# Optimization experiments

Hardware: AMD Instinct MI355X
Metric: run time of the kernel (lower is better)

## Reference

```python
import jax, jax.numpy as jnp
import numpy as np

N, IN_CAPS, OUT_CAPS, IN_LEN, OUT_LEN = 64, 256, 128, 16, 32
NUM_ITERATIONS = 3


def _squash(t, axis=-1):
    # scale * t / sqrt(||t||^2) with scale = ||t||^2 / (1 + ||t||^2)
    sq = jnp.sum(t * t, axis=axis, keepdims=True)
    return (sq / (1.0 + sq)) * t / jnp.sqrt(sq)


def setup_inputs() -> dict:
    key = jax.random.key(0)
    k1, k2 = jax.random.split(key)
    x = jax.random.normal(k1, (N, IN_CAPS, IN_LEN), dtype=jnp.float32)
    weight = jax.random.normal(k2, (OUT_CAPS, IN_CAPS, IN_LEN, OUT_LEN), dtype=jnp.float32)
    return {"x": x, "weight": weight}


def reference(x, weight):
    # priors: [out_caps, N, in_caps, out_len]  (torch keeps an extra singleton dim)
    priors = jnp.einsum('nik,oikl->onil', x, weight)
    logits = jnp.zeros_like(priors)
    outputs = None
    for i in range(NUM_ITERATIONS):
        # torch softmax(dim=2) == softmax over the in_caps axis
        probs = jax.nn.softmax(logits, axis=2)
        s = jnp.sum(probs * priors, axis=2, keepdims=True)  # [O, N, 1, L]
        outputs = _squash(s, axis=-1)
        if i != NUM_ITERATIONS - 1:
            # delta broadcasts over out_len, as in the torch code
            logits = logits + jnp.sum(priors * outputs, axis=-1, keepdims=True)
    # squeeze routing dim, transpose to [N, out_caps, out_len]
    return jnp.transpose(outputs[:, :, 0, :], (1, 0, 2))
```

## Files before the change

kernel.cpp:

```cpp
#include <hip/hip_runtime.h>


#define ICAPS 256
#define OCAPS 128
#define WS_WH 0ull
#define WS_WL 33554432ull
#define WS_XH 67108864ull
#define WS_XL 67633152ull
#define WS_NEED 68157440ull

typedef __attribute__((ext_vector_type(8))) short s16x8;
typedef __attribute__((ext_vector_type(16))) float f32x16;

__device__ inline unsigned bfbits(float f) {
    unsigned u = __float_as_uint(f);
    return (u + 0x7FFFu + ((u >> 16) & 1u)) & 0xFFFF0000u;
}

__global__ __launch_bounds__(256)
void caps_prep(const float* __restrict__ x, const float* __restrict__ w,
               unsigned char* __restrict__ ws) {
    const int wv = threadIdx.x >> 6, lane = threadIdx.x & 63;
    unsigned* WH = (unsigned*)(ws + WS_WH);
    unsigned* WL = (unsigned*)(ws + WS_WL);
    unsigned* XH = (unsigned*)(ws + WS_XH);
    unsigned* XL = (unsigned*)(ws + WS_XL);

    float f[8];
    if (blockIdx.x < 8192) {
        const int id = blockIdx.x * 4 + wv;
        const int l = lane & 31, kb = (lane >> 5) * 8;
        const float* src = w + ((size_t)id * 16 + kb) * 32 + l;
        #pragma unroll
        for (int j = 0; j < 8; ++j) f[j] = src[j * 32];
        unsigned h[4], g[4];
        #pragma unroll
        for (int c = 0; c < 4; ++c) {
            unsigned b0 = bfbits(f[2 * c]), b1 = bfbits(f[2 * c + 1]);
            h[c] = (b0 >> 16) | (b1 & 0xFFFF0000u);
            float l0 = f[2 * c] - __uint_as_float(b0);
            float l1 = f[2 * c + 1] - __uint_as_float(b1);
            g[c] = (bfbits(l0) >> 16) | (bfbits(l1) & 0xFFFF0000u);
        }
        const size_t o4 = (size_t)(id * 64 + lane) * 4;
        *(uint4*)(WH + o4) = make_uint4(h[0], h[1], h[2], h[3]);
        *(uint4*)(WL + o4) = make_uint4(g[0], g[1], g[2], g[3]);
    } else {
        const int id = (blockIdx.x - 8192) * 4 + wv;
        const int nh = id >> 8, i = id & 255;
        const int np = lane & 31, kb = (lane >> 5) * 8;
        const float* src = x + ((size_t)(nh * 32 + np) * ICAPS + i) * 16 + kb;
        float4 a = *(const float4*)src, b = *(const float4*)(src + 4);
        f[0] = a.x; f[1] = a.y; f[2] = a.z; f[3] = a.w;
        f[4] = b.x; f[5] = b.y; f[6] = b.z; f[7] = b.w;
        unsigned h[4], g[4];
        #pragma unroll
        for (int c = 0; c < 4; ++c) {
            unsigned b0 = bfbits(f[2 * c]), b1 = bfbits(f[2 * c + 1]);
            h[c] = (b0 >> 16) | (b1 & 0xFFFF0000u);
            float l0 = f[2 * c] - __uint_as_float(b0);
            float l1 = f[2 * c + 1] - __uint_as_float(b1);
            g[c] = (bfbits(l0) >> 16) | (bfbits(l1) & 0xFFFF0000u);
        }
        const size_t o4 = (size_t)(id * 64 + lane) * 4;
        *(uint4*)(XH + o4) = make_uint4(h[0], h[1], h[2], h[3]);
        *(uint4*)(XL + o4) = make_uint4(g[0], g[1], g[2], g[3]);
    }
}

__global__ __launch_bounds__(512)
void caps_main(const unsigned char* __restrict__ ws, float* __restrict__ out) {
    __shared__ float lg[ICAPS * 32];
    __shared__ float slab[8 * 1280];
    __shared__ float svv[32 * 33];
    __shared__ float zz[8 * 32];
    __shared__ float zinv[32];

    const int t = threadIdx.x, wv = t >> 6, lane = t & 63;
    const int o = blockIdx.x & 127, nh = blockIdx.x >> 7;
    const int n = lane & 31, half = lane >> 5;

    const s16x8* WHp = (const s16x8*)(ws + WS_WH) + (size_t)o * ICAPS * 64 + lane;
    const s16x8* WLp = (const s16x8*)(ws + WS_WL) + (size_t)o * ICAPS * 64 + lane;
    const s16x8* XHp = (const s16x8*)(ws + WS_XH) + (size_t)nh * ICAPS * 64 + lane;
    const s16x8* XLp = (const s16x8*)(ws + WS_XL) + (size_t)nh * ICAPS * 64 + lane;

    float vr[16];
    const int ibase = wv * 32;

    for (int pass = 0; pass < 3; ++pass) {
        float uacc[16];
        #pragma unroll
        for (int r = 0; r < 16; ++r) uacc[r] = 0.f;
        float z = 0.f;

        for (int ii = 0; ii < 32; ++ii) {
            const int i = ibase + ii;
            const s16x8 ah = WHp[(size_t)i * 64];
            const s16x8 al = WLp[(size_t)i * 64];
            const s16x8 bh = XHp[(size_t)i * 64];
            const s16x8 bl = XLp[(size_t)i * 64];
            f32x16 P = {};
            P = __builtin_amdgcn_mfma_f32_32x32x16_bf16(al, bh, P, 0, 0, 0);
            P = __builtin_amdgcn_mfma_f32_32x32x16_bf16(ah, bl, P, 0, 0, 0);
            P = __builtin_amdgcn_mfma_f32_32x32x16_bf16(ah, bh, P, 0, 0, 0);

            if (pass == 0) {
                #pragma unroll
                for (int r = 0; r < 16; ++r) uacc[r] += P[r];
            } else {
                float da = P[0] * vr[0];
                float db = P[8] * vr[8];
                #pragma unroll
                for (int r = 1; r < 8; ++r) {
                    da = fmaf(P[r], vr[r], da);
                    db = fmaf(P[r + 8], vr[r + 8], db);
                }
                float d = da + db;
                d += __shfl_xor(d, 32);
                if (pass == 1) {
                    if (half == 0) lg[i * 32 + n] = d;
                } else {
                    d += lg[i * 32 + n];
                }
                const float e = __expf(d);
                z += e;
                #pragma unroll
                for (int r = 0; r < 16; ++r) uacc[r] = fmaf(e, P[r], uacc[r]);
            }
        }

        #pragma unroll
        for (int c = 0; c < 4; ++c)
            *(float4*)(&slab[wv * 1280 + lane * 20 + c * 4]) =
                make_float4(uacc[4 * c], uacc[4 * c + 1], uacc[4 * c + 2], uacc[4 * c + 3]);
        if (pass > 0 && half == 0) zz[wv * 32 + n] = z;
        __syncthreads();

        #pragma unroll
        for (int hh = 0; hh < 2; ++hh) {
            const int e = t + hh * 512;
            const int lw = e >> 4, r = e & 15;
            float s = 0.f;
            #pragma unroll
            for (int w8 = 0; w8 < 8; ++w8) s += slab[w8 * 1280 + lw * 20 + r];
            const int nn = lw & 31, ll = (r & 3) + 8 * (r >> 2) + 4 * (lw >> 5);
            svv[nn * 33 + ll] = s;
        }
        if (t < 32) {
            if (pass == 0) zinv[t] = 1.0f / 256.0f;
            else {
                float zs = 0.f;
                #pragma unroll
                for (int w8 = 0; w8 < 8; ++w8) zs += zz[w8 * 32 + t];
                zinv[t] = 1.0f / zs;
            }
        }
        __syncthreads();

        {
            const int nq = t >> 4, sub = t & 15;
            const float a = svv[nq * 33 + sub] * zinv[nq];
            const float b = svv[nq * 33 + sub + 16] * zinv[nq];
            float sq = a * a + b * b;
            #pragma unroll
            for (int m = 1; m < 16; m <<= 1) sq += __shfl_xor(sq, m, 16);
            const float sc = sqrtf(sq) / (1.0f + sq);
            if (pass == 2) {
                const int ng = nh * 32 + nq;
                out[((size_t)ng * OCAPS + o) * 32 + sub] = a * sc;
                out[((size_t)ng * OCAPS + o) * 32 + sub + 16] = b * sc;
            } else {
                svv[nq * 33 + sub] = a * sc;
                svv[nq * 33 + sub + 16] = b * sc;
            }
        }
        if (pass < 2) {
            __syncthreads();
            #pragma unroll
            for (int r = 0; r < 16; ++r) {
                const int l = (r & 3) + 8 * (r >> 2) + 4 * half;
                vr[r] = svv[n * 33 + l];
            }
        }
    }
}

#define KLEN  16
#define LLEN  32
#define TN    16
#define LGS   257
#define XROW  20
#define XIST  (TN * XROW + 4)
#define SVS   33
#define RBS   33
#define NSTG  32
#define NSTEP (ICAPS / NSTG)

__global__ __launch_bounds__(512, 2)
void caps_route_fb(const float* __restrict__ xg_all,
                   const float* __restrict__ wg_all,
                   float* __restrict__ out) {
    __shared__ float lg[TN * LGS];
    __shared__ float xt[NSTG * XIST];
    __shared__ float sv[TN * SVS];
    __shared__ float zz[8][TN];
    __shared__ float zinv[TN];

    const int t   = threadIdx.x;
    const int o   = blockIdx.x & 127;
    const int n0  = (blockIdx.x >> 7) * TN;
    const int isp = t >> 4;
    const int lb  = (t >> 2) & 3;
    const int nb  = t & 3;
    const int l0  = lb * 8;

    const float* xg = xg_all + (size_t)n0 * ICAPS * KLEN;
    const float* wg = wg_all + (size_t)o * ICAPS * KLEN * LLEN;

    for (int pass = 0; pass < 3; ++pass) {
        float u[4][8];
        float zq[4] = {0.f, 0.f, 0.f, 0.f};
        #pragma unroll
        for (int q = 0; q < 4; ++q)
            #pragma unroll
            for (int r = 0; r < 8; ++r) u[q][r] = 0.f;

        for (int st = 0; st < NSTEP; ++st) {
            const int i0 = st * NSTG;
            __syncthreads();
            #pragma unroll
            for (int j = 0; j < 4; ++j) {
                const int g   = j * 512 + t;
                const int n   = g >> 7;
                const int rem = g & 127;
                const int il  = rem >> 2;
                const int k4c = rem & 3;
                *(float4*)(&xt[il * XIST + n * XROW + k4c * 4]) =
                    *(const float4*)(xg + (size_t)(n * ICAPS + i0 + il) * KLEN + k4c * 4);
            }
            __syncthreads();

            const int i = i0 + isp;
            const float* wp = wg + (size_t)i * (KLEN * LLEN) + l0;
            const float* xp = &xt[isp * XIST];
            float P[4][8];
            #pragma unroll
            for (int q = 0; q < 4; ++q)
                #pragma unroll
                for (int r = 0; r < 8; ++r) P[q][r] = 0.f;

            #pragma unroll
            for (int k4 = 0; k4 < 4; ++k4) {
                float xq[4][4];
                #pragma unroll
                for (int q = 0; q < 4; ++q)
                    *(float4*)(&xq[q][0]) = *(const float4*)(xp + (nb + 4 * q) * XROW + k4 * 4);
                #pragma unroll
                for (int kk = 0; kk < 4; ++kk) {
                    const int k = k4 * 4 + kk;
                    const float4 wa = *(const float4*)(wp + k * LLEN);
                    const float4 wb = *(const float4*)(wp + k * LLEN + 4);
                    #pragma unroll
                    for (int q = 0; q < 4; ++q) {
                        const float xv = xq[q][kk];
                        P[q][0] = fmaf(xv, wa.x, P[q][0]);
                        P[q][1] = fmaf(xv, wa.y, P[q][1]);
                        P[q][2] = fmaf(xv, wa.z, P[q][2]);
                        P[q][3] = fmaf(xv, wa.w, P[q][3]);
                        P[q][4] = fmaf(xv, wb.x, P[q][4]);
                        P[q][5] = fmaf(xv, wb.y, P[q][5]);
                        P[q][6] = fmaf(xv, wb.z, P[q][6]);
                        P[q][7] = fmaf(xv, wb.w, P[q][7]);
                    }
                }
            }

            if (pass == 0) {
                #pragma unroll
                for (int q = 0; q < 4; ++q)
                    #pragma unroll
                    for (int r = 0; r < 8; ++r) u[q][r] += P[q][r];
            } else {
                #pragma unroll
                for (int q = 0; q < 4; ++q) {
                    const float* vp = &sv[(nb + 4 * q) * SVS + l0];
                    float d = P[q][0] * vp[0] + P[q][1] * vp[1] + P[q][2] * vp[2] + P[q][3] * vp[3]
                            + P[q][4] * vp[4] + P[q][5] * vp[5] + P[q][6] * vp[6] + P[q][7] * vp[7];
                    d += __shfl_xor(d, 4);
                    d += __shfl_xor(d, 8);
                    float lnew = d;
                    if (pass == 2) lnew += lg[(nb + 4 * q) * LGS + i];
                    else if (lb == 0) lg[(nb + 4 * q) * LGS + i] = lnew;
                    const float e = __expf(lnew);
                    zq[q] += e;
                    #pragma unroll
                    for (int r = 0; r < 8; ++r) u[q][r] = fmaf(e, P[q][r], u[q][r]);
                }
            }
        }

        #pragma unroll
        for (int q = 0; q < 4; ++q) {
            #pragma unroll
            for (int r = 0; r < 8; ++r) {
                float v = u[q][r];
                v += __shfl_xor(v, 16);
                v += __shfl_xor(v, 32);
                u[q][r] = v;
            }
            float zv = zq[q];
            zv += __shfl_xor(zv, 16);
            zv += __shfl_xor(zv, 32);
            zq[q] = zv;
        }
        __syncthreads();
        {
            const int wvv = t >> 6, lane = t & 63;
            if (lane < 16) {
                float* rb = &xt[wvv * (16 * RBS) + lane * RBS];
                #pragma unroll
                for (int q = 0; q < 4; ++q)
                    #pragma unroll
                    for (int r = 0; r < 8; ++r) rb[q * 8 + r] = u[q][r];
            }
            if (pass > 0 && lane < 4) {
                #pragma unroll
                for (int q = 0; q < 4; ++q) zz[wvv][lane + 4 * q] = zq[q];
            }
        }
        __syncthreads();
        {
            const int low4 = t >> 5, qr = t & 31;
            const int qq = qr >> 3, rr = qr & 7;
            const int lbb = low4 >> 2, nbb = low4 & 3;
            float ssum = 0.f;
            #pragma unroll
            for (int w8 = 0; w8 < 8; ++w8) ssum += xt[w8 * (16 * RBS) + low4 * RBS + qr];
            sv[(nbb + 4 * qq) * SVS + lbb * 8 + rr] = ssum;
        }
        if (t < TN) {
            if (pass == 0) zinv[t] = 1.0f / 256.0f;
            else {
                float zs = 0.f;
                #pragma unroll
                for (int w8 = 0; w8 < 8; ++w8) zs += zz[w8][t];
                zinv[t] = 1.0f / zs;
            }
        }
        __syncthreads();
        {
            const int n = t >> 5, l = t & 31;
            const float val = sv[n * SVS + l] * zinv[n];
            float sq = val * val;
            #pragma unroll
            for (int m = 1; m < 32; m <<= 1) sq += __shfl_xor(sq, m, 32);
            const float sc = sqrtf(sq) / (1.0f + sq);
            if (pass == 2)
                out[((size_t)(n0 + n) * OCAPS + o) * LLEN + l] = val * sc;
            else
                sv[n * SVS + l] = val * sc;
        }
    }
}

extern "C" void kernel_launch(void* const* d_in, const int* in_sizes, int n_in,
                              void* d_out, int out_size, void* d_ws, size_t ws_size,
                              hipStream_t stream) {
    const float* x = (const float*)d_in[0];
    const float* w = (const float*)d_in[1];
    float* outp = (float*)d_out;
    if (ws_size >= WS_NEED) {
        caps_prep<<<dim3(8320), dim3(256), 0, stream>>>(x, w, (unsigned char*)d_ws);
        caps_main<<<dim3(256), dim3(512), 0, stream>>>((const unsigned char*)d_ws, outp);
    } else {
        caps_route_fb<<<dim3(512), dim3(512), 0, stream>>>(x, w, outp);
    }
}
```

Measured before the change: 151.4 us.

## Interleave hi/lo bf16 split storage and software-pipeline MFMA loads two caps per step

Stores the high and low bf16 halves of each weight and input fragment next to each other, so each lane fetches one contiguous 32-byte chunk instead of reading from two separate arrays. The main loop now processes two input capsules per iteration with two independent MFMA accumulator chains. It also prefetches the next pair's fragments into registers while the current MFMAs run, hiding global load latency. The prep kernel moves to 512-thread blocks. The costs are higher register use from the double buffers, which may lower occupancy, and pass 0 now reorders the fp32 summation.

```diff
diff --git a/kernel.cpp b/kernel.cpp
--- a/kernel.cpp
+++ b/kernel.cpp
@@ -3,10 +3,8 @@
 
 #define ICAPS 256
 #define OCAPS 128
-#define WS_WH 0ull
-#define WS_WL 33554432ull
-#define WS_XH 67108864ull
-#define WS_XL 67633152ull
+#define WS_WC 0ull
+#define WS_XC 67108864ull
 #define WS_NEED 68157440ull
 
 typedef __attribute__((ext_vector_type(8))) short s16x8;
@@ -17,20 +15,18 @@
     return (u + 0x7FFFu + ((u >> 16) & 1u)) & 0xFFFF0000u;
 }
 
-__global__ __launch_bounds__(256)
+__global__ __launch_bounds__(512)
 void caps_prep(const float* __restrict__ x, const float* __restrict__ w,
                unsigned char* __restrict__ ws) {
     const int wv = threadIdx.x >> 6, lane = threadIdx.x & 63;
-    unsigned* WH = (unsigned*)(ws + WS_WH);
-    unsigned* WL = (unsigned*)(ws + WS_WL);
-    unsigned* XH = (unsigned*)(ws + WS_XH);
-    unsigned* XL = (unsigned*)(ws + WS_XL);
+    uint4* WC = (uint4*)(ws + WS_WC);
+    uint4* XC = (uint4*)(ws + WS_XC);
+    const int gid = blockIdx.x * 8 + wv;
 
     float f[8];
-    if (blockIdx.x < 8192) {
-        const int id = blockIdx.x * 4 + wv;
+    if (gid < 32768) {
         const int l = lane & 31, kb = (lane >> 5) * 8;
-        const float* src = w + ((size_t)id * 16 + kb) * 32 + l;
+        const float* src = w + ((size_t)gid * 16 + kb) * 32 + l;
         #pragma unroll
         for (int j = 0; j < 8; ++j) f[j] = src[j * 32];
         unsigned h[4], g[4];
@@ -42,15 +38,16 @@
             float l1 = f[2 * c + 1] - __uint_as_float(b1);
             g[c] = (bfbits(l0) >> 16) | (bfbits(l1) & 0xFFFF0000u);
         }
-        const size_t o4 = (size_t)(id * 64 + lane) * 4;
-        *(uint4*)(WH + o4) = make_uint4(h[0], h[1], h[2], h[3]);
-        *(uint4*)(WL + o4) = make_uint4(g[0], g[1], g[2], g[3]);
+        const size_t idx = ((size_t)gid * 64 + lane) * 2;
+        WC[idx]     = make_uint4(h[0], h[1], h[2], h[3]);
+        WC[idx + 1] = make_uint4(g[0], g[1], g[2], g[3]);
     } else {
-        const int id = (blockIdx.x - 8192) * 4 + wv;
+        const int id = gid - 32768;
         const int nh = id >> 8, i = id & 255;
         const int np = lane & 31, kb = (lane >> 5) * 8;
         const float* src = x + ((size_t)(nh * 32 + np) * ICAPS + i) * 16 + kb;
-        float4 a = *(const float4*)src, b = *(const float4*)(src + 4);
+        const float4 a = *(const float4*)src;
+        const float4 b = *(const float4*)(src + 4);
         f[0] = a.x; f[1] = a.y; f[2] = a.z; f[3] = a.w;
         f[4] = b.x; f[5] = b.y; f[6] = b.z; f[7] = b.w;
         unsigned h[4], g[4];
@@ -62,9 +59,9 @@
             float l1 = f[2 * c + 1] - __uint_as_float(b1);
             g[c] = (bfbits(l0) >> 16) | (bfbits(l1) & 0xFFFF0000u);
         }
-        const size_t o4 = (size_t)(id * 64 + lane) * 4;
-        *(uint4*)(XH + o4) = make_uint4(h[0], h[1], h[2], h[3]);
-        *(uint4*)(XL + o4) = make_uint4(g[0], g[1], g[2], g[3]);
+        const size_t idx = ((size_t)id * 64 + lane) * 2;
+        XC[idx]     = make_uint4(h[0], h[1], h[2], h[3]);
+        XC[idx + 1] = make_uint4(g[0], g[1], g[2], g[3]);
     }
 }
 
@@ -80,10 +77,8 @@
     const int o = blockIdx.x & 127, nh = blockIdx.x >> 7;
     const int n = lane & 31, half = lane >> 5;
 
-    const s16x8* WHp = (const s16x8*)(ws + WS_WH) + (size_t)o * ICAPS * 64 + lane;
-    const s16x8* WLp = (const s16x8*)(ws + WS_WL) + (size_t)o * ICAPS * 64 + lane;
-    const s16x8* XHp = (const s16x8*)(ws + WS_XH) + (size_t)nh * ICAPS * 64 + lane;
-    const s16x8* XLp = (const s16x8*)(ws + WS_XL) + (size_t)nh * ICAPS * 64 + lane;
+    const s16x8* Wp = (const s16x8*)(ws + WS_WC) + ((size_t)o * ICAPS * 64 + lane) * 2;
+    const s16x8* Xp = (const s16x8*)(ws + WS_XC) + ((size_t)nh * ICAPS * 64 + lane) * 2;
 
     float vr[16];
     const int ibase = wv * 32;
@@ -94,39 +89,82 @@
         for (int r = 0; r < 16; ++r) uacc[r] = 0.f;
         float z = 0.f;
 
-        for (int ii = 0; ii < 32; ++ii) {
-            const int i = ibase + ii;
-            const s16x8 ah = WHp[(size_t)i * 64];
-            const s16x8 al = WLp[(size_t)i * 64];
-            const s16x8 bh = XHp[(size_t)i * 64];
-            const s16x8 bl = XLp[(size_t)i * 64];
-            f32x16 P = {};
-            P = __builtin_amdgcn_mfma_f32_32x32x16_bf16(al, bh, P, 0, 0, 0);
-            P = __builtin_amdgcn_mfma_f32_32x32x16_bf16(ah, bl, P, 0, 0, 0);
-            P = __builtin_amdgcn_mfma_f32_32x32x16_bf16(ah, bh, P, 0, 0, 0);
-
-            if (pass == 0) {
-                #pragma unroll
-                for (int r = 0; r < 16; ++r) uacc[r] += P[r];
-            } else {
-                float da = P[0] * vr[0];
-                float db = P[8] * vr[8];
-                #pragma unroll
-                for (int r = 1; r < 8; ++r) {
-                    da = fmaf(P[r], vr[r], da);
-                    db = fmaf(P[r + 8], vr[r + 8], db);
-                }
-                float d = da + db;
-                d += __shfl_xor(d, 32);
-                if (pass == 1) {
-                    if (half == 0) lg[i * 32 + n] = d;
-                } else {
-                    d += lg[i * 32 + n];
-                }
-                const float e = __expf(d);
-                z += e;
-                #pragma unroll
-                for (int r = 0; r < 16; ++r) uacc[r] = fmaf(e, P[r], uacc[r]);
+        s16x8 C[8], Nx[8];
+        {
+            const size_t b0 = (size_t)ibase * 128;
+            C[0] = Wp[b0];       C[1] = Wp[b0 + 1];
+            C[2] = Xp[b0];       C[3] = Xp[b0 + 1];
+            C[4] = Wp[b0 + 128]; C[5] = Wp[b0 + 129];
+            C[6] = Xp[b0 + 128]; C[7] = Xp[b0 + 129];
+        }
+
+        if (pass == 0) {
+            f32x16 Pa = {}, Pb = {};
+            for (int bb = 0; bb < 16; ++bb) {
+                if (bb < 15) {
+                    const size_t bn = (size_t)(ibase + 2 * (bb + 1)) * 128;
+                    Nx[0] = Wp[bn];       Nx[1] = Wp[bn + 1];
+                    Nx[2] = Xp[bn];       Nx[3] = Xp[bn + 1];
+                    Nx[4] = Wp[bn + 128]; Nx[5] = Wp[bn + 129];
+                    Nx[6] = Xp[bn + 128]; Nx[7] = Xp[bn + 129];
+                }
+                Pa = __builtin_amdgcn_mfma_f32_32x32x16_bf16(C[1], C[2], Pa, 0, 0, 0);
+                Pb = __builtin_amdgcn_mfma_f32_32x32x16_bf16(C[5], C[6], Pb, 0, 0, 0);
+                Pa = __builtin_amdgcn_mfma_f32_32x32x16_bf16(C[0], C[3], Pa, 0, 0, 0);
+                Pb = __builtin_amdgcn_mfma_f32_32x32x16_bf16(C[4], C[7], Pb, 0, 0, 0);
+                Pa = __builtin_amdgcn_mfma_f32_32x32x16_bf16(C[0], C[2], Pa, 0, 0, 0);
+                Pb = __builtin_amdgcn_mfma_f32_32x32x16_bf16(C[4], C[6], Pb, 0, 0, 0);
+                if (bb < 15) {
+                    #pragma unroll
+                    for (int j = 0; j < 8; ++j) C[j] = Nx[j];
+                }
+            }
+            #pragma unroll
+            for (int r = 0; r < 16; ++r) uacc[r] = Pa[r] + Pb[r];
+        } else {
+            for (int bb = 0; bb < 16; ++bb) {
+                if (bb < 15) {
+                    const size_t bn = (size_t)(ibase + 2 * (bb + 1)) * 128;
+                    Nx[0] = Wp[bn];       Nx[1] = Wp[bn + 1];
+                    Nx[2] = Xp[bn];       Nx[3] = Xp[bn + 1];
+                    Nx[4] = Wp[bn + 128]; Nx[5] = Wp[bn + 129];
+                    Nx[6] = Xp[bn + 128]; Nx[7] = Xp[bn + 129];
+                }
+                f32x16 P0 = {}, P1 = {};
+                P0 = __builtin_amdgcn_mfma_f32_32x32x16_bf16(C[1], C[2], P0, 0, 0, 0);
+                P1 = __builtin_amdgcn_mfma_f32_32x32x16_bf16(C[5], C[6], P1, 0, 0, 0);
+                P0 = __builtin_amdgcn_mfma_f32_32x32x16_bf16(C[0], C[3], P0, 0, 0, 0);
+                P1 = __builtin_amdgcn_mfma_f32_32x32x16_bf16(C[4], C[7], P1, 0, 0, 0);
+                P0 = __builtin_amdgcn_mfma_f32_32x32x16_bf16(C[0], C[2], P0, 0, 0, 0);
+                P1 = __builtin_amdgcn_mfma_f32_32x32x16_bf16(C[4], C[6], P1, 0, 0, 0);
+
+                #pragma unroll
+                for (int j = 0; j < 2; ++j) {
+                    const f32x16& P = j ? P1 : P0;
+                    const int i = ibase + bb * 2 + j;
+                    float da = P[0] * vr[0];
+                    float db = P[8] * vr[8];
+                    #pragma unroll
+                    for (int r = 1; r < 8; ++r) {
+                        da = fmaf(P[r], vr[r], da);
+                        db = fmaf(P[r + 8], vr[r + 8], db);
+                    }
+                    float d = da + db;
+                    d += __shfl_xor(d, 32);
+                    if (pass == 1) {
+                        if (half == 0) lg[i * 32 + n] = d;
+                    } else {
+                        d += lg[i * 32 + n];
+                    }
+                    const float e = __expf(d);
+                    z += e;
+                    #pragma unroll
+                    for (int r = 0; r < 16; ++r) uacc[r] = fmaf(e, P[r], uacc[r]);
+                }
+                if (bb < 15) {
+                    #pragma unroll
+                    for (int j = 0; j < 8; ++j) C[j] = Nx[j];
+                }
             }
         }
 
@@ -232,12 +270,12 @@
             #pragma unroll
             for (int j = 0; j < 4; ++j) {
                 const int g   = j * 512 + t;
-                const int n   = g >> 7;
+                const int nn  = g >> 7;
                 const int rem = g & 127;
                 const int il  = rem >> 2;
                 const int k4c = rem & 3;
-                *(float4*)(&xt[il * XIST + n * XROW + k4c * 4]) =
-                    *(const float4*)(xg + (size_t)(n * ICAPS + i0 + il) * KLEN + k4c * 4);
+                *(float4*)(&xt[il * XIST + nn * XROW + k4c * 4]) =
+                    *(const float4*)(xg + (size_t)(nn * ICAPS + i0 + il) * KLEN + k4c * 4);
             }
             __syncthreads();
 
@@ -350,16 +388,16 @@
         }
         __syncthreads();
         {
-            const int n = t >> 5, l = t & 31;
-            const float val = sv[n * SVS + l] * zinv[n];
+            const int nn = t >> 5, l = t & 31;
+            const float val = sv[nn * SVS + l] * zinv[nn];
             float sq = val * val;
             #pragma unroll
             for (int m = 1; m < 32; m <<= 1) sq += __shfl_xor(sq, m, 32);
             const float sc = sqrtf(sq) / (1.0f + sq);
             if (pass == 2)
-                out[((size_t)(n0 + n) * OCAPS + o) * LLEN + l] = val * sc;
+                out[((size_t)(n0 + nn) * OCAPS + o) * LLEN + l] = val * sc;
             else
-                sv[n * SVS + l] = val * sc;
+                sv[nn * SVS + l] = val * sc;
         }
     }
 }
@@ -371,7 +409,7 @@
     const float* w = (const float*)d_in[1];
     float* outp = (float*)d_out;
     if (ws_size >= WS_NEED) {
-        caps_prep<<<dim3(8320), dim3(256), 0, stream>>>(x, w, (unsigned char*)d_ws);
+        caps_prep<<<dim3(4160), dim3(512), 0, stream>>>(x, w, (unsigned char*)d_ws);
         caps_main<<<dim3(256), dim3(512), 0, stream>>>((const unsigned char*)d_ws, outp);
     } else {
         caps_route_fb<<<dim3(512), dim3(512), 0, stream>>>(x, w, outp);
```

Result: no change. 151.5 us (+0.1%).

## Split weights to bf16 hi/lo inside main kernel, drop weight prep pass

Applied to the files above, without the earlier changes.

Removes the separate pass that converted the 64MB fp32 weight tensor into bf16 hi/lo workspace arrays. The main kernel now reads fp32 weights directly, splits them in registers with truncation and byte-perm, and double-buffers loads over groups of four input capsules. Only x is still pre-split, into a single interleaved buffer. Pass 0 now accumulates into two MFMA accumulators and launch bounds request two blocks per CU. The cost is that weights are re-read and re-split in every routing pass (3x fp32 reads), more register pressure, and the hi part uses truncation instead of round-to-nearest.

```diff
diff --git a/kernel.cpp b/kernel.cpp
--- a/kernel.cpp
+++ b/kernel.cpp
@@ -3,73 +3,52 @@
 
 #define ICAPS 256
 #define OCAPS 128
-#define WS_WH 0ull
-#define WS_WL 33554432ull
-#define WS_XH 67108864ull
-#define WS_XL 67633152ull
-#define WS_NEED 68157440ull
+#define WS_NEED 1048576ull
 
 typedef __attribute__((ext_vector_type(8))) short s16x8;
 typedef __attribute__((ext_vector_type(16))) float f32x16;
 
-__device__ inline unsigned bfbits(float f) {
-    unsigned u = __float_as_uint(f);
-    return (u + 0x7FFFu + ((u >> 16) & 1u)) & 0xFFFF0000u;
-}
-
-__global__ __launch_bounds__(256)
-void caps_prep(const float* __restrict__ x, const float* __restrict__ w,
-               unsigned char* __restrict__ ws) {
+union u4s8 { unsigned u[4]; s16x8 v; };
+
+__device__ inline void split8(const float* f, s16x8& hi, s16x8& lo) {
+    u4s8 H, L;
+    #pragma unroll
+    for (int c = 0; c < 4; ++c) {
+        const unsigned u0 = __float_as_uint(f[2 * c]);
+        const unsigned u1 = __float_as_uint(f[2 * c + 1]);
+        H.u[c] = __builtin_amdgcn_perm(u1, u0, 0x07060302u);
+        const float h0 = __uint_as_float(u0 & 0xFFFF0000u);
+        const float h1 = __uint_as_float(u1 & 0xFFFF0000u);
+        const unsigned l0 = __float_as_uint(f[2 * c] - h0);
+        const unsigned l1 = __float_as_uint(f[2 * c + 1] - h1);
+        L.u[c] = __builtin_amdgcn_perm(l1, l0, 0x07060302u);
+    }
+    hi = H.v; lo = L.v;
+}
+
+__global__ __launch_bounds__(512)
+void caps_prep_x(const float* __restrict__ x, unsigned char* __restrict__ ws) {
     const int wv = threadIdx.x >> 6, lane = threadIdx.x & 63;
-    unsigned* WH = (unsigned*)(ws + WS_WH);
-    unsigned* WL = (unsigned*)(ws + WS_WL);
-    unsigned* XH = (unsigned*)(ws + WS_XH);
-    unsigned* XL = (unsigned*)(ws + WS_XL);
-
+    const int id = blockIdx.x * 8 + wv;
+    const int nh = id >> 8, i = id & 255;
+    const int np = lane & 31, kb = (lane >> 5) * 8;
+    const float* src = x + ((size_t)(nh * 32 + np) * ICAPS + i) * 16 + kb;
     float f[8];
-    if (blockIdx.x < 8192) {
-        const int id = blockIdx.x * 4 + wv;
-        const int l = lane & 31, kb = (lane >> 5) * 8;
-        const float* src = w + ((size_t)id * 16 + kb) * 32 + l;
-        #pragma unroll
-        for (int j = 0; j < 8; ++j) f[j] = src[j * 32];
-        unsigned h[4], g[4];
-        #pragma unroll
-        for (int c = 0; c < 4; ++c) {
-            unsigned b0 = bfbits(f[2 * c]), b1 = bfbits(f[2 * c + 1]);
-            h[c] = (b0 >> 16) | (b1 & 0xFFFF0000u);
-            float l0 = f[2 * c] - __uint_as_float(b0);
-            float l1 = f[2 * c + 1] - __uint_as_float(b1);
-            g[c] = (bfbits(l0) >> 16) | (bfbits(l1) & 0xFFFF0000u);
-        }
-        const size_t o4 = (size_t)(id * 64 + lane) * 4;
-        *(uint4*)(WH + o4) = make_uint4(h[0], h[1], h[2], h[3]);
-        *(uint4*)(WL + o4) = make_uint4(g[0], g[1], g[2], g[3]);
-    } else {
-        const int id = (blockIdx.x - 8192) * 4 + wv;
-        const int nh = id >> 8, i = id & 255;
-        const int np = lane & 31, kb = (lane >> 5) * 8;
-        const float* src = x + ((size_t)(nh * 32 + np) * ICAPS + i) * 16 + kb;
-        float4 a = *(const float4*)src, b = *(const float4*)(src + 4);
-        f[0] = a.x; f[1] = a.y; f[2] = a.z; f[3] = a.w;
-        f[4] = b.x; f[5] = b.y; f[6] = b.z; f[7] = b.w;
-        unsigned h[4], g[4];
-        #pragma unroll
-        for (int c = 0; c < 4; ++c) {
-            unsigned b0 = bfbits(f[2 * c]), b1 = bfbits(f[2 * c + 1]);
-            h[c] = (b0 >> 16) | (b1 & 0xFFFF0000u);
-            float l0 = f[2 * c] - __uint_as_float(b0);
-            float l1 = f[2 * c + 1] - __uint_as_float(b1);
-            g[c] = (bfbits(l0) >> 16) | (bfbits(l1) & 0xFFFF0000u);
-        }
-        const size_t o4 = (size_t)(id * 64 + lane) * 4;
-        *(uint4*)(XH + o4) = make_uint4(h[0], h[1], h[2], h[3]);
-        *(uint4*)(XL + o4) = make_uint4(g[0], g[1], g[2], g[3]);
-    }
-}
-
-__global__ __launch_bounds__(512)
-void caps_main(const unsigned char* __restrict__ ws, float* __restrict__ out) {
+    const float4 a = *(const float4*)src;
+    const float4 b = *(const float4*)(src + 4);
+    f[0] = a.x; f[1] = a.y; f[2] = a.z; f[3] = a.w;
+    f[4] = b.x; f[5] = b.y; f[6] = b.z; f[7] = b.w;
+    s16x8 hi, lo;
+    split8(f, hi, lo);
+    s16x8* XC = (s16x8*)ws;
+    const size_t idx = ((size_t)id * 64 + lane) * 2;
+    XC[idx] = hi;
+    XC[idx + 1] = lo;
+}
+
+__global__ __launch_bounds__(512, 2)
+void caps_main(const float* __restrict__ w, const unsigned char* __restrict__ ws,
+               float* __restrict__ out) {
     __shared__ float lg[ICAPS * 32];
     __shared__ float slab[8 * 1280];
     __shared__ float svv[32 * 33];
@@ -80,35 +59,60 @@
     const int o = blockIdx.x & 127, nh = blockIdx.x >> 7;
     const int n = lane & 31, half = lane >> 5;
 
-    const s16x8* WHp = (const s16x8*)(ws + WS_WH) + (size_t)o * ICAPS * 64 + lane;
-    const s16x8* WLp = (const s16x8*)(ws + WS_WL) + (size_t)o * ICAPS * 64 + lane;
-    const s16x8* XHp = (const s16x8*)(ws + WS_XH) + (size_t)nh * ICAPS * 64 + lane;
-    const s16x8* XLp = (const s16x8*)(ws + WS_XL) + (size_t)nh * ICAPS * 64 + lane;
+    const float* wg = w + (size_t)o * (ICAPS * 512) + (lane >> 5) * 256 + (lane & 31);
+    const s16x8* Xp = (const s16x8*)ws + ((size_t)nh * ICAPS * 64 + lane) * 2;
 
     float vr[16];
     const int ibase = wv * 32;
 
+    auto LOADB = [&](int ib, float (&Wb)[4][8], s16x8 (&Xb)[4][2]) {
+        #pragma unroll
+        for (int j = 0; j < 4; ++j) {
+            const float* wp = wg + (size_t)(ib + j) * 512;
+            #pragma unroll
+            for (int k = 0; k < 8; ++k) Wb[j][k] = wp[k * 32];
+            Xb[j][0] = Xp[(size_t)(ib + j) * 128];
+            Xb[j][1] = Xp[(size_t)(ib + j) * 128 + 1];
+        }
+    };
+
     for (int pass = 0; pass < 3; ++pass) {
         float uacc[16];
         #pragma unroll
         for (int r = 0; r < 16; ++r) uacc[r] = 0.f;
         float z = 0.f;
 
-        for (int ii = 0; ii < 32; ++ii) {
-            const int i = ibase + ii;
-            const s16x8 ah = WHp[(size_t)i * 64];
-            const s16x8 al = WLp[(size_t)i * 64];
-            const s16x8 bh = XHp[(size_t)i * 64];
-            const s16x8 bl = XLp[(size_t)i * 64];
-            f32x16 P = {};
-            P = __builtin_amdgcn_mfma_f32_32x32x16_bf16(al, bh, P, 0, 0, 0);
-            P = __builtin_amdgcn_mfma_f32_32x32x16_bf16(ah, bl, P, 0, 0, 0);
-            P = __builtin_amdgcn_mfma_f32_32x32x16_bf16(ah, bh, P, 0, 0, 0);
-
-            if (pass == 0) {
-                #pragma unroll
-                for (int r = 0; r < 16; ++r) uacc[r] += P[r];
-            } else {
+        float W0[4][8], W1[4][8];
+        s16x8 X0[4][2], X1[4][2];
+        f32x16 Pa = {}, Pb = {};
+
+        auto PROC0 = [&](float (&Wb)[4][8], s16x8 (&Xb)[4][2]) {
+            #pragma unroll
+            for (int j = 0; j < 4; ++j) {
+                s16x8 ah, al;
+                split8(Wb[j], ah, al);
+                if (j & 1) {
+                    Pb = __builtin_amdgcn_mfma_f32_32x32x16_bf16(al, Xb[j][0], Pb, 0, 0, 0);
+                    Pb = __builtin_amdgcn_mfma_f32_32x32x16_bf16(ah, Xb[j][1], Pb, 0, 0, 0);
+                    Pb = __builtin_amdgcn_mfma_f32_32x32x16_bf16(ah, Xb[j][0], Pb, 0, 0, 0);
+                } else {
+                    Pa = __builtin_amdgcn_mfma_f32_32x32x16_bf16(al, Xb[j][0], Pa, 0, 0, 0);
+                    Pa = __builtin_amdgcn_mfma_f32_32x32x16_bf16(ah, Xb[j][1], Pa, 0, 0, 0);
+                    Pa = __builtin_amdgcn_mfma_f32_32x32x16_bf16(ah, Xb[j][0], Pa, 0, 0, 0);
+                }
+            }
+        };
+
+        auto PROC12 = [&](int ib, float (&Wb)[4][8], s16x8 (&Xb)[4][2]) {
+            #pragma unroll
+            for (int j = 0; j < 4; ++j) {
+                s16x8 ah, al;
+                split8(Wb[j], ah, al);
+                f32x16 P = {};
+                P = __builtin_amdgcn_mfma_f32_32x32x16_bf16(al, Xb[j][0], P, 0, 0, 0);
+                P = __builtin_amdgcn_mfma_f32_32x32x16_bf16(ah, Xb[j][1], P, 0, 0, 0);
+                P = __builtin_amdgcn_mfma_f32_32x32x16_bf16(ah, Xb[j][0], P, 0, 0, 0);
+                const int i = ib + j;
                 float da = P[0] * vr[0];
                 float db = P[8] * vr[8];
                 #pragma unroll
@@ -128,6 +132,20 @@
                 #pragma unroll
                 for (int r = 0; r < 16; ++r) uacc[r] = fmaf(e, P[r], uacc[r]);
             }
+        };
+
+        LOADB(ibase, W0, X0);
+        for (int bb = 0; bb < 8; bb += 2) {
+            if (bb + 1 < 8) LOADB(ibase + (bb + 1) * 4, W1, X1);
+            if (pass == 0) PROC0(W0, X0); else PROC12(ibase + bb * 4, W0, X0);
+            if (bb + 2 < 8) LOADB(ibase + (bb + 2) * 4, W0, X0);
+            if (bb + 1 < 8) {
+                if (pass == 0) PROC0(W1, X1); else PROC12(ibase + (bb + 1) * 4, W1, X1);
+            }
+        }
+        if (pass == 0) {
+            #pragma unroll
+            for (int r = 0; r < 16; ++r) uacc[r] = Pa[r] + Pb[r];
         }
 
         #pragma unroll
@@ -232,12 +250,12 @@
             #pragma unroll
             for (int j = 0; j < 4; ++j) {
                 const int g   = j * 512 + t;
-                const int n   = g >> 7;
+                const int nn  = g >> 7;
                 const int rem = g & 127;
                 const int il  = rem >> 2;
                 const int k4c = rem & 3;
-                *(float4*)(&xt[il * XIST + n * XROW + k4c * 4]) =
-                    *(const float4*)(xg + (size_t)(n * ICAPS + i0 + il) * KLEN + k4c * 4);
+                *(float4*)(&xt[il * XIST + nn * XROW + k4c * 4]) =
+                    *(const float4*)(xg + (size_t)(nn * ICAPS + i0 + il) * KLEN + k4c * 4);
             }
             __syncthreads();
 
@@ -350,16 +368,16 @@
         }
         __syncthreads();
         {
-            const int n = t >> 5, l = t & 31;
-            const float val = sv[n * SVS + l] * zinv[n];
+            const int nn = t >> 5, l = t & 31;
+            const float val = sv[nn * SVS + l] * zinv[nn];
             float sq = val * val;
             #pragma unroll
             for (int m = 1; m < 32; m <<= 1) sq += __shfl_xor(sq, m, 32);
             const float sc = sqrtf(sq) / (1.0f + sq);
             if (pass == 2)
-                out[((size_t)(n0 + n) * OCAPS + o) * LLEN + l] = val * sc;
+                out[((size_t)(n0 + nn) * OCAPS + o) * LLEN + l] = val * sc;
             else
-                sv[n * SVS + l] = val * sc;
+                sv[nn * SVS + l] = val * sc;
         }
     }
 }
@@ -371,8 +389,8 @@
     const float* w = (const float*)d_in[1];
     float* outp = (float*)d_out;
     if (ws_size >= WS_NEED) {
-        caps_prep<<<dim3(8320), dim3(256), 0, stream>>>(x, w, (unsigned char*)d_ws);
-        caps_main<<<dim3(256), dim3(512), 0, stream>>>((const unsigned char*)d_ws, outp);
+        caps_prep_x<<<dim3(64), dim3(512), 0, stream>>>(x, (unsigned char*)d_ws);
+        caps_main<<<dim3(256), dim3(512), 0, stream>>>(w, (const unsigned char*)d_ws, outp);
     } else {
         caps_route_fb<<<dim3(512), dim3(512), 0, stream>>>(x, w, outp);
     }
```

Result: slower. 269.8 us (+78.2%).
